# Optimization experiments

Measured on AMD Instinct MI355X. Metric: run time of the kernel, lower is better.

## Reference

```python
import jax, jax.numpy as jnp
import numpy as np

B, L, C, H = 32, 512, 512, 8
DH = C // H
LN_EPS = 1e-5


def setup_inputs() -> dict:
    key = jax.random.key(0)
    ks = jax.random.split(key, 5)
    x = jax.random.normal(ks[0], (B, L, C), dtype=jnp.float32)
    # nn.Linear weights are (out, in); y = x @ W.T
    wq = jax.random.normal(ks[1], (C, C), dtype=jnp.float32) * 0.02
    wk = jax.random.normal(ks[2], (C, C), dtype=jnp.float32) * 0.02
    wv = jax.random.normal(ks[3], (C, C), dtype=jnp.float32) * 0.02
    # source zero-inits the bias table; use small randoms so it actually contributes
    bias_table = jax.random.normal(ks[4], (2 * L - 1, H), dtype=jnp.float32) * 0.02
    gamma = jnp.ones((C,), dtype=jnp.float32)
    beta = jnp.zeros((C,), dtype=jnp.float32)
    coords = np.arange(L)
    rel_index = jnp.asarray(coords[None, :] - coords[:, None] + (L - 1), dtype=jnp.int32)  # (L, L)
    return {"x": x, "wq": wq, "wk": wk, "wv": wv, "bias_table": bias_table,
            "gamma": gamma, "beta": beta, "rel_index": rel_index}


def reference(x, wq, wk, wv, bias_table, gamma, beta, rel_index):
    Bx, Lx, Cx = x.shape
    scale = Cx ** (-0.5)  # note: scale uses full emb_size, as in source
    q = (x @ wq.T).reshape(Bx, Lx, H, DH).transpose(0, 2, 1, 3)  # (B,H,L,Dh)
    k = (x @ wk.T).reshape(Bx, Lx, H, DH).transpose(0, 2, 1, 3)
    v = (x @ wv.T).reshape(Bx, Lx, H, DH).transpose(0, 2, 1, 3)
    attn = jax.nn.softmax(jnp.einsum('bhqd,bhkd->bhqk', q, k) * scale, axis=-1)
    # post-softmax relative bias gather-add
    rel_bias = bias_table[rel_index]                # (L, L, H)
    attn = attn + rel_bias.transpose(2, 0, 1)[None]  # (1,H,L,L) broadcast
    out = jnp.einsum('bhqk,bhkd->bhqd', attn, v)
    out = out.transpose(0, 2, 1, 3).reshape(Bx, Lx, Cx)
    mu = out.mean(axis=-1, keepdims=True)
    var = jnp.mean(jnp.square(out - mu), axis=-1, keepdims=True)
    return gamma * (out - mu) * jax.lax.rsqrt(var + LN_EPS) + beta
```

## Files before the change

### kernel.cpp

```cpp
#include <hip/hip_runtime.h>
#include <hip/hip_bf16.h>

typedef unsigned short u16;
typedef __attribute__((ext_vector_type(8))) __bf16 bf16x8;
typedef __attribute__((ext_vector_type(4))) float f32x4;
typedef __attribute__((ext_vector_type(4))) unsigned int u32x4;

#define BB 32
#define LL 512
#define CC 512
#define HH 8
#define DH 64
#define MROWS (BB * LL)
#define NQKV  (3 * CC)

#define XB_BYTES ((size_t)MROWS * CC * 2)
#define WC_BYTES ((size_t)NQKV * CC * 2)
#define QKV_OFF  (XB_BYTES + WC_BYTES)

#define SCALE2 (0.044194173824159216f * 1.4426950408889634f)

__device__ inline u16 f2b(float f) {
  union { float f; unsigned u; } a; a.f = f;
  unsigned u = a.u;
  return (u16)((u + 0x7FFFu + ((u >> 16) & 1u)) >> 16);
}

__device__ inline unsigned pack2(float a, float b) {
  float2 f; f.x = a; f.y = b;
  union { __hip_bfloat162 h; unsigned u; } c;
  c.h = __float22bfloat162_rn(f);
  return c.u;
}

__global__ __launch_bounds__(256) void cvt_x(const float* __restrict__ x, u16* __restrict__ xb) {
  int i = blockIdx.x * 256 + threadIdx.x;
  float4 v = ((const float4*)x)[i];
  uint2 o; o.x = pack2(v.x, v.y); o.y = pack2(v.z, v.w);
  ((uint2*)xb)[i] = o;
}

__global__ __launch_bounds__(256) void cvt_w(const float* __restrict__ wq, const float* __restrict__ wk,
                                             const float* __restrict__ wv, u16* __restrict__ wcat) {
  int i = blockIdx.x * 256 + threadIdx.x;
  int e = i * 4;
  int n = e >> 9;
  int k = e & 511;
  const float* src = (n < 512) ? (wq + (size_t)n * 512)
                   : (n < 1024) ? (wk + (size_t)(n - 512) * 512)
                                : (wv + (size_t)(n - 1024) * 512);
  const float sc = (n < 512) ? SCALE2 : 1.0f;
  float4 v = *(const float4*)(src + k);
  uint2 o; o.x = pack2(v.x * sc, v.y * sc); o.y = pack2(v.z * sc, v.w * sc);
  *(uint2*)(wcat + (size_t)n * 512 + k) = o;
}

typedef __attribute__((address_space(1))) void* as1_void_p;
typedef __attribute__((address_space(3))) void* as3_void_p;

__device__ inline void async16(const u16* g, u16* l) {
#if __has_builtin(__builtin_amdgcn_global_load_lds)
  __builtin_amdgcn_global_load_lds((as1_void_p)g, (as3_void_p)l, 16, 0, 0);
#else
  *(uint4*)l = *(const uint4*)g;
#endif
}

__global__ __launch_bounds__(256) void gemm_qkv(const u16* __restrict__ A, const u16* __restrict__ Bw,
                                                u16* __restrict__ Cm) {
  __shared__ u16 a_lds[128 * 32];
  __shared__ u16 b_lds[128 * 32];
  const int n0 = blockIdx.x * 128, m0 = blockIdx.y * 128;
  const int t = threadIdx.x, l = t & 63;
  const int wrow = ((t >> 7) & 1) * 64, wcol = ((t >> 6) & 1) * 64;
  const int lr = l & 15, lq = l >> 4;

  f32x4 acc[4][4] = {};

  for (int k0 = 0; k0 < 512; k0 += 32) {
    {
      int c0 = t, c1 = t + 256;
      async16(A  + (size_t)(m0 + (c0 >> 2)) * 512 + k0 + (c0 & 3) * 8, &a_lds[c0 * 8]);
      async16(A  + (size_t)(m0 + (c1 >> 2)) * 512 + k0 + (c1 & 3) * 8, &a_lds[c1 * 8]);
      async16(Bw + (size_t)(n0 + (c0 >> 2)) * 512 + k0 + (c0 & 3) * 8, &b_lds[c0 * 8]);
      async16(Bw + (size_t)(n0 + (c1 >> 2)) * 512 + k0 + (c1 & 3) * 8, &b_lds[c1 * 8]);
    }
    __syncthreads();
    bf16x8 af[4], bfr[4];
#pragma unroll
    for (int r = 0; r < 4; ++r) af[r]  = *(const bf16x8*)&a_lds[(wrow + r * 16 + lr) * 32 + lq * 8];
#pragma unroll
    for (int c = 0; c < 4; ++c) bfr[c] = *(const bf16x8*)&b_lds[(wcol + c * 16 + lr) * 32 + lq * 8];
#pragma unroll
    for (int r = 0; r < 4; ++r)
#pragma unroll
      for (int c = 0; c < 4; ++c)
        acc[r][c] = __builtin_amdgcn_mfma_f32_16x16x32_bf16(af[r], bfr[c], acc[r][c], 0, 0, 0);
    __syncthreads();
  }
#pragma unroll
  for (int r = 0; r < 4; ++r) {
#pragma unroll
    for (int i = 0; i < 4; ++i) {
      int m = m0 + wrow + r * 16 + lq * 4 + i;
      u16* crow = Cm + (size_t)m * NQKV + n0 + wcol;
#pragma unroll
      for (int c = 0; c < 4; ++c)
        crow[c * 16 + lr] = f2b(acc[r][c][i]);
    }
  }
}

__global__ __launch_bounds__(256) void transpose_v(const u16* __restrict__ qkv, u16* __restrict__ vT,
                                                   const float* __restrict__ bias_table,
                                                   float* __restrict__ biasT) {
  if (blockIdx.y == 4) {
    if (blockIdx.x < 32) {
      int i = blockIdx.x * 256 + threadIdx.x;
      if (i < 1023 * 8) {
        float v = bias_table[i];
        int rel = i >> 3, hh = i & 7;
        biasT[hh * 1024 + rel] = v;
      }
    }
    return;
  }
  const int bh = blockIdx.x;
  const int b = bh >> 3, h = bh & 7;
  const int lc0 = blockIdx.y * 128;
  __shared__ u16 tile[32 * 72];
  const int t = threadIdx.x;
  for (int lc = lc0; lc < lc0 + 128; lc += 32) {
    int lrow = t >> 3, dcol = (t & 7) * 8;
    const u16* src = qkv + (size_t)(b * 512 + lc + lrow) * NQKV + 1024 + h * 64 + dcol;
    *(uint4*)&tile[lrow * 72 + dcol] = *(const uint4*)src;
    __syncthreads();
    int d = t >> 2, lp = (t & 3) * 8;
    union { ushort4 v4[2]; u16 s[8]; } tmp;
#pragma unroll
    for (int j = 0; j < 8; ++j) tmp.s[j] = tile[(lp + j) * 72 + d];
    *(uint4*)&vT[(size_t)(bh * 64 + d) * 512 + lc + lp] = *(uint4*)&tmp;
    __syncthreads();
  }
}

__global__ __launch_bounds__(256, 3) void attn_kernel(const u16* __restrict__ qkv, const u16* __restrict__ vT,
                                                      const float* __restrict__ biasT,
                                                      float* __restrict__ out) {
  __shared__ u16 p_lds[32 * 512];
  __shared__ float bias_lds[544];
  __shared__ float reds[4][32];

  const int flat = blockIdx.x;
  const int bh = ((flat >> 7) << 3) | (flat & 7);
  const int q0 = ((flat >> 3) & 15) * 32;
  const int b = bh >> 3, h = bh & 7;
  const int t = threadIdx.x, l = t & 63, w = t >> 6;
  const int lr = l & 15, lq = l >> 4;

  {
    const int rel0 = 480 - q0;
    const float* bsrc = biasT + h * 1024 + rel0;
    for (int i = t; i < 543; i += 256)
      bias_lds[i] = bsrc[i];
  }

  bf16x8 bq[2][2];
#pragma unroll
  for (int qt = 0; qt < 2; ++qt) {
    const u16* qrow = qkv + (size_t)(b * 512 + q0 + qt * 16 + lr) * NQKV + h * 64;
    bq[qt][0] = *(const bf16x8*)(qrow + lq * 8);
    bq[qt][1] = *(const bf16x8*)(qrow + 32 + lq * 8);
  }

  const u16* kbase = qkv + (size_t)(b * 512 + w * 128 + lr) * NQKV + 512 + h * 64 + lq * 8;
  u32x4 akr[8][2];
#pragma unroll
  for (int ct = 0; ct < 8; ++ct) {
    const u16* kr = kbase + (size_t)ct * 16 * NQKV;
    asm volatile("global_load_dwordx4 %0, %2, off\n\t"
                 "global_load_dwordx4 %1, %2, off offset:64"
                 : "=&v"(akr[ct][0]), "=&v"(akr[ct][1]) : "v"(kr));
  }
  asm volatile("s_waitcnt vmcnt(0)" ::: "memory");
  __builtin_amdgcn_sched_barrier(0);

  f32x4 sT[2][8];
  __builtin_amdgcn_s_setprio(1);
#pragma unroll
  for (int ct = 0; ct < 8; ++ct) {
    bf16x8 ak0 = __builtin_bit_cast(bf16x8, akr[ct][0]);
    bf16x8 ak1 = __builtin_bit_cast(bf16x8, akr[ct][1]);
    f32x4 a0 = {0.f, 0.f, 0.f, 0.f}, a1 = {0.f, 0.f, 0.f, 0.f};
    a0 = __builtin_amdgcn_mfma_f32_16x16x32_bf16(ak0, bq[0][0], a0, 0, 0, 0);
    a0 = __builtin_amdgcn_mfma_f32_16x16x32_bf16(ak1, bq[0][1], a0, 0, 0, 0);
    a1 = __builtin_amdgcn_mfma_f32_16x16x32_bf16(ak0, bq[1][0], a1, 0, 0, 0);
    a1 = __builtin_amdgcn_mfma_f32_16x16x32_bf16(ak1, bq[1][1], a1, 0, 0, 0);
    sT[0][ct] = a0;
    sT[1][ct] = a1;
  }
  __builtin_amdgcn_s_setprio(0);

  float sq[2];
#pragma unroll
  for (int qt = 0; qt < 2; ++qt) {
    float s0 = 0.f, s1 = 0.f, s2 = 0.f, s3 = 0.f;
#pragma unroll
    for (int ct = 0; ct < 8; ++ct) {
      float e0 = exp2f(sT[qt][ct][0]);
      float e1 = exp2f(sT[qt][ct][1]);
      float e2 = exp2f(sT[qt][ct][2]);
      float e3 = exp2f(sT[qt][ct][3]);
      sT[qt][ct][0] = e0; sT[qt][ct][1] = e1;
      sT[qt][ct][2] = e2; sT[qt][ct][3] = e3;
      s0 += e0; s1 += e1; s2 += e2; s3 += e3;
    }
    sq[qt] = (s0 + s1) + (s2 + s3);
  }
  {
    float t0 = sq[0], t1 = sq[1];
    float u0 = __shfl_xor(t0, 16, 64), u1 = __shfl_xor(t1, 16, 64);
    t0 += u0; t1 += u1;
    u0 = __shfl_xor(t0, 32, 64); u1 = __shfl_xor(t1, 32, 64);
    sq[0] = t0 + u0; sq[1] = t1 + u1;
  }
  if (lq == 0) { reds[w][lr] = sq[0]; reds[w][16 + lr] = sq[1]; }
  __syncthreads();
  float rinv[2];
#pragma unroll
  for (int qt = 0; qt < 2; ++qt)
    rinv[qt] = 1.0f / (reds[0][qt * 16 + lr] + reds[1][qt * 16 + lr] +
                       reds[2][qt * 16 + lr] + reds[3][qt * 16 + lr]);

  const u16* vrow = vT + (size_t)(bh * 64 + w * 16 + lr) * 512 + lq * 8;
  u32x4 avr[16];
#define GLV(i, o0, o1)                                                         \
  asm volatile("global_load_dwordx4 %0, %2, off offset:" o0 "\n\t"             \
               "global_load_dwordx4 %1, %2, off offset:" o1                    \
               : "=&v"(avr[i]), "=&v"(avr[(i) + 1]) : "v"(vrow))
  GLV(0, "0", "64"); GLV(2, "128", "192"); GLV(4, "256", "320"); GLV(6, "384", "448");

#define PACK_QT(qt)                                                            \
  {                                                                            \
    const int qlocal = (qt) * 16 + lr;                                         \
    u16* prow = p_lds + qlocal * 512;                                          \
    const int boff = w * 128 + lq * 4 + 31 - qlocal;                           \
    _Pragma("unroll")                                                          \
    for (int ct = 0; ct < 8; ++ct) {                                           \
      const int gsw = w * 8 + (ct ^ (lr & 7));                                 \
      float p0 = sT[qt][ct][0] * rinv[qt] + bias_lds[boff + ct * 16 + 0];      \
      float p1 = sT[qt][ct][1] * rinv[qt] + bias_lds[boff + ct * 16 + 1];      \
      float p2 = sT[qt][ct][2] * rinv[qt] + bias_lds[boff + ct * 16 + 2];      \
      float p3 = sT[qt][ct][3] * rinv[qt] + bias_lds[boff + ct * 16 + 3];      \
      uint2 pk; pk.x = pack2(p0, p1); pk.y = pack2(p2, p3);                    \
      *(uint2*)&prow[gsw * 16 + lq * 4] = pk;                                  \
    }                                                                          \
  }

  PACK_QT(0)
  GLV(8, "512", "576"); GLV(10, "640", "704"); GLV(12, "768", "832"); GLV(14, "896", "960");
#undef GLV
  PACK_QT(1)
#undef PACK_QT

  __syncthreads();
  asm volatile("s_waitcnt vmcnt(0)" ::: "memory");
  __builtin_amdgcn_sched_barrier(0);

  f32x4 accP[2] = {};
  bf16x8 bp[4][2];
#define LDP(kb, qt) \
  (*(const bf16x8*)&p_lds[((qt) * 16 + lr) * 512 + \
    (((2 * (kb) + (lq >> 1)) & ~7) | (((2 * (kb) + (lq >> 1)) & 7) ^ (lr & 7))) * 16 + (lq & 1) * 8])
#pragma unroll
  for (int pre = 0; pre < 3; ++pre) { bp[pre][0] = LDP(pre, 0); bp[pre][1] = LDP(pre, 1); }
  __builtin_amdgcn_s_setprio(1);
#pragma unroll
  for (int kb = 0; kb < 16; ++kb) {
    if (kb < 13) {
      bp[(kb + 3) & 3][0] = LDP(kb + 3, 0);
      bp[(kb + 3) & 3][1] = LDP(kb + 3, 1);
    }
    bf16x8 av = __builtin_bit_cast(bf16x8, avr[kb]);
    accP[0] = __builtin_amdgcn_mfma_f32_16x16x32_bf16(av, bp[kb & 3][0], accP[0], 0, 0, 0);
    accP[1] = __builtin_amdgcn_mfma_f32_16x16x32_bf16(av, bp[kb & 3][1], accP[1], 0, 0, 0);
  }
  __builtin_amdgcn_s_setprio(0);
#undef LDP
#pragma unroll
  for (int qt = 0; qt < 2; ++qt)
    *(f32x4*)&out[(size_t)(b * 512 + q0 + qt * 16 + lr) * 512 + h * 64 + w * 16 + lq * 4] = accP[qt];
}

__global__ __launch_bounds__(256) void ln_kernel(float* __restrict__ out,
                                                 const float* __restrict__ gamma,
                                                 const float* __restrict__ beta) {
  const int t = threadIdx.x;
  const int r2 = t >> 7;
  const int row = blockIdx.x * 2 + r2;
  const int c = (t & 127) * 4;
  float* p = out + (size_t)row * 512;
  float4 v = *(float4*)(p + c);
  float s = v.x + v.y + v.z + v.w;
  float s2 = v.x * v.x + v.y * v.y + v.z * v.z + v.w * v.w;
#pragma unroll
  for (int d = 1; d < 64; d <<= 1) { s += __shfl_xor(s, d, 64); s2 += __shfl_xor(s2, d, 64); }
  __shared__ float ps[4], ps2[4];
  const int wv = t >> 6;
  if ((t & 63) == 0) { ps[wv] = s; ps2[wv] = s2; }
  __syncthreads();
  s  = ps[r2 * 2]  + ps[r2 * 2 + 1];
  s2 = ps2[r2 * 2] + ps2[r2 * 2 + 1];
  float mu = s * (1.0f / 512.0f);
  float var = s2 * (1.0f / 512.0f) - mu * mu;
  float rs = rsqrtf(var + 1e-5f);
  float4 g = *(const float4*)(gamma + c);
  float4 bb = *(const float4*)(beta + c);
  v.x = g.x * (v.x - mu) * rs + bb.x;
  v.y = g.y * (v.y - mu) * rs + bb.y;
  v.z = g.z * (v.z - mu) * rs + bb.z;
  v.w = g.w * (v.w - mu) * rs + bb.w;
  *(float4*)(p + c) = v;
}

extern "C" void kernel_launch(void* const* d_in, const int* in_sizes, int n_in,
                              void* d_out, int out_size, void* d_ws, size_t ws_size,
                              hipStream_t stream) {
  const float* x    = (const float*)d_in[0];
  const float* wq   = (const float*)d_in[1];
  const float* wk   = (const float*)d_in[2];
  const float* wv   = (const float*)d_in[3];
  const float* bias = (const float*)d_in[4];
  const float* gamma = (const float*)d_in[5];
  const float* beta  = (const float*)d_in[6];
  float* out = (float*)d_out;

  char* ws = (char*)d_ws;
  u16* xb   = (u16*)ws;
  u16* wcat = (u16*)(ws + XB_BYTES);
  u16* qkv  = (u16*)(ws + QKV_OFF);
  u16* vT   = xb;
  float* biasT = (float*)(ws + XB_BYTES);

  cvt_x<<<dim3((MROWS * CC) / 4 / 256), 256, 0, stream>>>(x, xb);
  cvt_w<<<dim3((NQKV * CC) / 4 / 256), 256, 0, stream>>>(wq, wk, wv, wcat);
  gemm_qkv<<<dim3(NQKV / 128, MROWS / 128), 256, 0, stream>>>(xb, wcat, qkv);
  transpose_v<<<dim3(256, 5), 256, 0, stream>>>(qkv, vT, bias, biasT);
  attn_kernel<<<dim3(16 * 256), 256, 0, stream>>>(qkv, vT, biasT, out);
  ln_kernel<<<dim3(MROWS / 2), 256, 0, stream>>>(out, gamma, beta);
}
```

Before: 227.0 us.

## Stream K and V loads through rotating register buffers to raise attention occupancy

Replaces the upfront load of all K and V fragments with small rotating register buffers and explicit vmcnt waits, so loads overlap the MFMAs while fewer VGPRs are live. This allows the launch bound to move from 3 to 4 waves per SIMD. It also swaps exp2f and the division for the hardware exp2 and reciprocal builtins, and replaces __syncthreads with a raw barrier plus lgkmcnt wait. The gain depends on whether the extra occupancy outweighs the shallower prefetch. It relies on hand-counted vmcnt values, which break if the compiler emits other vector memory ops in between.

```diff
diff --git a/kernel.cpp b/kernel.cpp
--- a/kernel.cpp
+++ b/kernel.cpp
@@ -19,6 +19,17 @@
 #define QKV_OFF  (XB_BYTES + WC_BYTES)
 
 #define SCALE2 (0.044194173824159216f * 1.4426950408889634f)
+
+#if __has_builtin(__builtin_amdgcn_exp2f)
+#define EXP2(x) __builtin_amdgcn_exp2f(x)
+#else
+#define EXP2(x) exp2f(x)
+#endif
+#if __has_builtin(__builtin_amdgcn_rcpf)
+#define RCP(x) __builtin_amdgcn_rcpf(x)
+#else
+#define RCP(x) (1.0f / (x))
+#endif
 
 __device__ inline u16 f2b(float f) {
   union { float f; unsigned u; } a; a.f = f;
@@ -144,7 +155,7 @@
   }
 }
 
-__global__ __launch_bounds__(256, 3) void attn_kernel(const u16* __restrict__ qkv, const u16* __restrict__ vT,
+__global__ __launch_bounds__(256, 4) void attn_kernel(const u16* __restrict__ qkv, const u16* __restrict__ vT,
                                                       const float* __restrict__ biasT,
                                                       float* __restrict__ out) {
   __shared__ u16 p_lds[32 * 512];
@@ -164,6 +175,7 @@
     for (int i = t; i < 543; i += 256)
       bias_lds[i] = bsrc[i];
   }
+  asm volatile("s_waitcnt vmcnt(0)" ::: "memory");
 
   bf16x8 bq[2][2];
 #pragma unroll
@@ -174,32 +186,31 @@
   }
 
   const u16* kbase = qkv + (size_t)(b * 512 + w * 128 + lr) * NQKV + 512 + h * 64 + lq * 8;
-  u32x4 akr[8][2];
-#pragma unroll
-  for (int ct = 0; ct < 8; ++ct) {
-    const u16* kr = kbase + (size_t)ct * 16 * NQKV;
-    asm volatile("global_load_dwordx4 %0, %2, off\n\t"
-                 "global_load_dwordx4 %1, %2, off offset:64"
-                 : "=&v"(akr[ct][0]), "=&v"(akr[ct][1]) : "v"(kr));
-  }
-  asm volatile("s_waitcnt vmcnt(0)" ::: "memory");
-  __builtin_amdgcn_sched_barrier(0);
-
+  u32x4 akr[4][2];
   f32x4 sT[2][8];
-  __builtin_amdgcn_s_setprio(1);
-#pragma unroll
-  for (int ct = 0; ct < 8; ++ct) {
-    bf16x8 ak0 = __builtin_bit_cast(bf16x8, akr[ct][0]);
-    bf16x8 ak1 = __builtin_bit_cast(bf16x8, akr[ct][1]);
-    f32x4 a0 = {0.f, 0.f, 0.f, 0.f}, a1 = {0.f, 0.f, 0.f, 0.f};
-    a0 = __builtin_amdgcn_mfma_f32_16x16x32_bf16(ak0, bq[0][0], a0, 0, 0, 0);
-    a0 = __builtin_amdgcn_mfma_f32_16x16x32_bf16(ak1, bq[0][1], a0, 0, 0, 0);
-    a1 = __builtin_amdgcn_mfma_f32_16x16x32_bf16(ak0, bq[1][0], a1, 0, 0, 0);
-    a1 = __builtin_amdgcn_mfma_f32_16x16x32_bf16(ak1, bq[1][1], a1, 0, 0, 0);
-    sT[0][ct] = a0;
-    sT[1][ct] = a1;
-  }
-  __builtin_amdgcn_s_setprio(0);
+
+#define KISSUE(slot, ct) { const u16* kr = kbase + (size_t)(ct) * 16 * NQKV;   \
+    asm volatile("global_load_dwordx4 %0, %2, off\n\t"                         \
+                 "global_load_dwordx4 %1, %2, off offset:64"                   \
+                 : "=&v"(akr[slot][0]), "=&v"(akr[slot][1]) : "v"(kr)); }
+#define KSTEP(ct, lit, doissue) {                                              \
+    if (doissue) KISSUE(((ct) + 3) & 3, (ct) + 3)                              \
+    asm volatile("s_waitcnt vmcnt(" lit ")"                                    \
+                 : "+v"(akr[(ct) & 3][0]), "+v"(akr[(ct) & 3][1]));            \
+    bf16x8 ak0 = __builtin_bit_cast(bf16x8, akr[(ct) & 3][0]);                 \
+    bf16x8 ak1 = __builtin_bit_cast(bf16x8, akr[(ct) & 3][1]);                 \
+    f32x4 a0 = {0.f, 0.f, 0.f, 0.f}, a1 = {0.f, 0.f, 0.f, 0.f};                \
+    a0 = __builtin_amdgcn_mfma_f32_16x16x32_bf16(ak0, bq[0][0], a0, 0, 0, 0);  \
+    a0 = __builtin_amdgcn_mfma_f32_16x16x32_bf16(ak1, bq[0][1], a0, 0, 0, 0);  \
+    a1 = __builtin_amdgcn_mfma_f32_16x16x32_bf16(ak0, bq[1][0], a1, 0, 0, 0);  \
+    a1 = __builtin_amdgcn_mfma_f32_16x16x32_bf16(ak1, bq[1][1], a1, 0, 0, 0);  \
+    sT[0][ct] = a0; sT[1][ct] = a1; }
+
+  KISSUE(0, 0) KISSUE(1, 1) KISSUE(2, 2)
+  KSTEP(0, "6", 1) KSTEP(1, "6", 1) KSTEP(2, "6", 1) KSTEP(3, "6", 1)
+  KSTEP(4, "6", 1) KSTEP(5, "4", 0) KSTEP(6, "2", 0) KSTEP(7, "0", 0)
+#undef KSTEP
+#undef KISSUE
 
   float sq[2];
 #pragma unroll
@@ -207,10 +218,10 @@
     float s0 = 0.f, s1 = 0.f, s2 = 0.f, s3 = 0.f;
 #pragma unroll
     for (int ct = 0; ct < 8; ++ct) {
-      float e0 = exp2f(sT[qt][ct][0]);
-      float e1 = exp2f(sT[qt][ct][1]);
-      float e2 = exp2f(sT[qt][ct][2]);
-      float e3 = exp2f(sT[qt][ct][3]);
+      float e0 = EXP2(sT[qt][ct][0]);
+      float e1 = EXP2(sT[qt][ct][1]);
+      float e2 = EXP2(sT[qt][ct][2]);
+      float e3 = EXP2(sT[qt][ct][3]);
       sT[qt][ct][0] = e0; sT[qt][ct][1] = e1;
       sT[qt][ct][2] = e2; sT[qt][ct][3] = e3;
       s0 += e0; s1 += e1; s2 += e2; s3 += e3;
@@ -225,20 +236,24 @@
     sq[0] = t0 + u0; sq[1] = t1 + u1;
   }
   if (lq == 0) { reds[w][lr] = sq[0]; reds[w][16 + lr] = sq[1]; }
-  __syncthreads();
+
+  asm volatile("s_waitcnt lgkmcnt(0)" ::: "memory");
+  __builtin_amdgcn_s_barrier();
+  asm volatile("" ::: "memory");
+
   float rinv[2];
 #pragma unroll
   for (int qt = 0; qt < 2; ++qt)
-    rinv[qt] = 1.0f / (reds[0][qt * 16 + lr] + reds[1][qt * 16 + lr] +
-                       reds[2][qt * 16 + lr] + reds[3][qt * 16 + lr]);
+    rinv[qt] = RCP(reds[0][qt * 16 + lr] + reds[1][qt * 16 + lr] +
+                   reds[2][qt * 16 + lr] + reds[3][qt * 16 + lr]);
 
   const u16* vrow = vT + (size_t)(bh * 64 + w * 16 + lr) * 512 + lq * 8;
-  u32x4 avr[16];
-#define GLV(i, o0, o1)                                                         \
-  asm volatile("global_load_dwordx4 %0, %2, off offset:" o0 "\n\t"             \
-               "global_load_dwordx4 %1, %2, off offset:" o1                    \
-               : "=&v"(avr[i]), "=&v"(avr[(i) + 1]) : "v"(vrow))
-  GLV(0, "0", "64"); GLV(2, "128", "192"); GLV(4, "256", "320"); GLV(6, "384", "448");
+  u32x4 avr[8];
+#define VISSUE(slot, olit)                                                     \
+  asm volatile("global_load_dwordx4 %0, %1, off offset:" olit                  \
+               : "=&v"(avr[slot]) : "v"(vrow));
+  VISSUE(0, "0")   VISSUE(1, "64")  VISSUE(2, "128") VISSUE(3, "192")
+  VISSUE(4, "256") VISSUE(5, "320") VISSUE(6, "384") VISSUE(7, "448")
 
 #define PACK_QT(qt)                                                            \
   {                                                                            \
@@ -256,36 +271,41 @@
       *(uint2*)&prow[gsw * 16 + lq * 4] = pk;                                  \
     }                                                                          \
   }
-
   PACK_QT(0)
-  GLV(8, "512", "576"); GLV(10, "640", "704"); GLV(12, "768", "832"); GLV(14, "896", "960");
-#undef GLV
   PACK_QT(1)
 #undef PACK_QT
 
-  __syncthreads();
-  asm volatile("s_waitcnt vmcnt(0)" ::: "memory");
-  __builtin_amdgcn_sched_barrier(0);
+  asm volatile("s_waitcnt lgkmcnt(0)" ::: "memory");
+  __builtin_amdgcn_s_barrier();
+  asm volatile("" ::: "memory");
 
   f32x4 accP[2] = {};
-  bf16x8 bp[4][2];
+  bf16x8 bp[2][2];
 #define LDP(kb, qt) \
   (*(const bf16x8*)&p_lds[((qt) * 16 + lr) * 512 + \
     (((2 * (kb) + (lq >> 1)) & ~7) | (((2 * (kb) + (lq >> 1)) & 7) ^ (lr & 7))) * 16 + (lq & 1) * 8])
-#pragma unroll
-  for (int pre = 0; pre < 3; ++pre) { bp[pre][0] = LDP(pre, 0); bp[pre][1] = LDP(pre, 1); }
-  __builtin_amdgcn_s_setprio(1);
-#pragma unroll
-  for (int kb = 0; kb < 16; ++kb) {
-    if (kb < 13) {
-      bp[(kb + 3) & 3][0] = LDP(kb + 3, 0);
-      bp[(kb + 3) & 3][1] = LDP(kb + 3, 1);
-    }
-    bf16x8 av = __builtin_bit_cast(bf16x8, avr[kb]);
-    accP[0] = __builtin_amdgcn_mfma_f32_16x16x32_bf16(av, bp[kb & 3][0], accP[0], 0, 0, 0);
-    accP[1] = __builtin_amdgcn_mfma_f32_16x16x32_bf16(av, bp[kb & 3][1], accP[1], 0, 0, 0);
-  }
-  __builtin_amdgcn_s_setprio(0);
+  bp[0][0] = LDP(0, 0);
+  bp[0][1] = LDP(0, 1);
+#define PVSTEP(kb, lit, doissue, olit) {                                       \
+    asm volatile("s_waitcnt vmcnt(" lit ")" : "+v"(avr[(kb) & 7]));            \
+    if ((kb) < 15) {                                                           \
+      bp[((kb) + 1) & 1][0] = LDP((kb) + 1, 0);                                \
+      bp[((kb) + 1) & 1][1] = LDP((kb) + 1, 1);                                \
+    }                                                                          \
+    bf16x8 av = __builtin_bit_cast(bf16x8, avr[(kb) & 7]);                     \
+    accP[0] = __builtin_amdgcn_mfma_f32_16x16x32_bf16(av, bp[(kb) & 1][0], accP[0], 0, 0, 0); \
+    accP[1] = __builtin_amdgcn_mfma_f32_16x16x32_bf16(av, bp[(kb) & 1][1], accP[1], 0, 0, 0); \
+    if (doissue) VISSUE((kb) & 7, olit) }
+  PVSTEP(0,  "7", 1, "512") PVSTEP(1,  "7", 1, "576")
+  PVSTEP(2,  "7", 1, "640") PVSTEP(3,  "7", 1, "704")
+  PVSTEP(4,  "7", 1, "768") PVSTEP(5,  "7", 1, "832")
+  PVSTEP(6,  "7", 1, "896") PVSTEP(7,  "7", 1, "960")
+  PVSTEP(8,  "7", 0, "0")   PVSTEP(9,  "6", 0, "0")
+  PVSTEP(10, "5", 0, "0")   PVSTEP(11, "4", 0, "0")
+  PVSTEP(12, "3", 0, "0")   PVSTEP(13, "2", 0, "0")
+  PVSTEP(14, "1", 0, "0")   PVSTEP(15, "0", 0, "0")
+#undef PVSTEP
+#undef VISSUE
 #undef LDP
 #pragma unroll
   for (int qt = 0; qt < 2; ++qt)
```

Result: no change. 224.3 us (-1.2%).
